# Kernel optimization log

Hardware: AMD Instinct MI355X
Metric: run time of the kernel (lower is better)

The kernel has to match this reference:

```python
import jax, jax.numpy as jnp
import numpy as np

N = 100000
E = 1600000
DIMS = [128, 128, 64]


def _gcn_norm(edge_index, num_nodes):
    # PyG gcn_norm: add self-loops, symmetric normalization D^-1/2 (A+I) D^-1/2
    src, dst = edge_index[0], edge_index[1]
    loop = jnp.arange(num_nodes, dtype=src.dtype)
    src = jnp.concatenate([src, loop])
    dst = jnp.concatenate([dst, loop])
    deg = jax.ops.segment_sum(jnp.ones_like(src, dtype=jnp.float32), dst,
                              num_segments=num_nodes)
    dinv = jnp.where(deg > 0, jax.lax.rsqrt(deg), 0.0)
    w = dinv[src] * dinv[dst]  # [E+N]
    return src, dst, w


def _gcn_conv(x, src, dst, w, W, b):
    # transform first (cheaper when out_dim <= in_dim), then aggregate
    h = x @ W                                   # [N, out]
    msg = h[src] * w[:, None]                   # gather + scale  [E+N, out]
    out = jax.ops.segment_sum(msg, dst, num_segments=x.shape[0])
    return out + b


def setup_inputs() -> dict:
    key = jax.random.key(0)
    ks = jax.random.split(key, 6)
    x = jax.random.normal(ks[0], (N, DIMS[0]), dtype=jnp.float32)
    edge_index = jax.random.randint(ks[1], (2, E), 0, N, dtype=jnp.int64)
    # Glorot-style init for GCNConv weights, zero bias (PyG default)
    W1 = jax.random.normal(ks[2], (DIMS[0], DIMS[1]), dtype=jnp.float32) / np.sqrt(DIMS[0])
    b1 = jnp.zeros((DIMS[1],), dtype=jnp.float32)
    W2 = jax.random.normal(ks[3], (DIMS[1], DIMS[2]), dtype=jnp.float32) / np.sqrt(DIMS[1])
    b2 = jnp.zeros((DIMS[2],), dtype=jnp.float32)
    return {"x": x, "edge_index": edge_index, "W1": W1, "b1": b1, "W2": W2, "b2": b2}


def reference(x, edge_index, W1, b1, W2, b2):
    src, dst, w = _gcn_norm(edge_index, x.shape[0])
    h = _gcn_conv(x, src, dst, w, W1, b1)
    h = jax.nn.relu(h)
    # dropout is identity in eval mode (deterministic reference)
    out = _gcn_conv(h, src, dst, w, W2, b2)
    return out
```

## Files before the change

### kernel.cpp

```cpp
#include <hip/hip_runtime.h>
#include <hip/hip_fp16.h>

#define TPB 256
#define CHUNK 1024
#define EPB 4096
#define CSHIFT 8

typedef _Float16 half8 __attribute__((ext_vector_type(8)));
typedef float    f32x4 __attribute__((ext_vector_type(4)));


__global__ __launch_bounds__(256) void scanA_kernel(const int* __restrict__ cnt,
                                                    int* __restrict__ row_ptr,
                                                    int* __restrict__ chunk_sums, int n) {
    __shared__ int ls[256];
    const int t    = threadIdx.x;
    const int base = blockIdx.x * CHUNK;
    const int idx  = base + t * 4;
    int4 v = make_int4(0, 0, 0, 0);
    if (idx + 3 < n) v = *(const int4*)(cnt + idx);
    else {
        if (idx + 0 < n) v.x = cnt[idx + 0];
        if (idx + 1 < n) v.y = cnt[idx + 1];
        if (idx + 2 < n) v.z = cnt[idx + 2];
        if (idx + 3 < n) v.w = cnt[idx + 3];
    }
    int s0 = v.x, s1 = s0 + v.y, s2 = s1 + v.z, s3 = s2 + v.w;
    ls[t] = s3;
    __syncthreads();
    for (int off = 1; off < 256; off <<= 1) {
        int xv = (t >= off) ? ls[t - off] : 0;
        __syncthreads();
        ls[t] += xv;
        __syncthreads();
    }
    int excl = (t == 0) ? 0 : ls[t - 1];
    if (idx + 0 < n) row_ptr[idx + 0] = excl;
    if (idx + 1 < n) row_ptr[idx + 1] = excl + s0;
    if (idx + 2 < n) row_ptr[idx + 2] = excl + s1;
    if (idx + 3 < n) row_ptr[idx + 3] = excl + s2;
    if (t == 255) chunk_sums[blockIdx.x] = ls[255];
}

__global__ __launch_bounds__(256) void scanB_kernel(int* __restrict__ chunk_sums, int nch) {
    __shared__ int ls[256];
    const int t = threadIdx.x;
    ls[t] = (t < nch) ? chunk_sums[t] : 0;
    __syncthreads();
    for (int off = 1; off < 256; off <<= 1) {
        int xv = (t >= off) ? ls[t - off] : 0;
        __syncthreads();
        ls[t] += xv;
        __syncthreads();
    }
    if (t < nch) chunk_sums[t] = (t == 0) ? 0 : ls[t - 1];
}

__global__ __launch_bounds__(256) void scanC_kernel(int* __restrict__ row_ptr,
                                                    const int* __restrict__ chunk_sums, int n) {
    const int base = blockIdx.x * CHUNK;
    const int off  = chunk_sums[blockIdx.x];
    for (int k = threadIdx.x; k < CHUNK; k += 256) {
        int i = base + k;
        if (i < n) row_ptr[i] += off;
    }
}


__global__ __launch_bounds__(256) void hist_kernel(const int* __restrict__ dst,
                                                   int* __restrict__ hist_g,
                                                   int e, int nbc, int nblk) {
    __shared__ int hs[512];
    const int t = threadIdx.x;
    for (int i = t; i < nbc; i += 256) hs[i] = 0;
    __syncthreads();
    const int e0  = blockIdx.x * EPB;
    const int lim = min(e0 + EPB, e);
    for (int i = e0 + t; i < lim; i += 256)
        atomicAdd(&hs[dst[i] >> CSHIFT], 1);
    __syncthreads();
    for (int b = t; b < nbc; b += 256)
        hist_g[b * nblk + blockIdx.x] = hs[b];
}

__global__ __launch_bounds__(256) void partition_kernel(const int* __restrict__ src,
                                                        const int* __restrict__ dst,
                                                        const int* __restrict__ hist_scan,
                                                        int* __restrict__ pairs,
                                                        int e, int nbc, int nblk) {
    __shared__ int  hs[512];
    __shared__ int  lscan[512];
    __shared__ int  lfill[512];
    __shared__ int  base_s[512];
    __shared__ int  ls[256];
    __shared__ int2 sp[EPB];
    const int t = threadIdx.x;
    for (int i = t; i < nbc; i += 256) { hs[i] = 0; lfill[i] = 0; }
    __syncthreads();
    const int e0  = blockIdx.x * EPB;
    const int lim = min(e0 + EPB, e);
    for (int i = e0 + t; i < lim; i += 256)
        atomicAdd(&hs[dst[i] >> CSHIFT], 1);
    __syncthreads();
    int v0 = (2 * t     < nbc) ? hs[2 * t]     : 0;
    int v1 = (2 * t + 1 < nbc) ? hs[2 * t + 1] : 0;
    ls[t] = v0 + v1;
    __syncthreads();
    for (int off = 1; off < 256; off <<= 1) {
        int xv = (t >= off) ? ls[t - off] : 0;
        __syncthreads();
        ls[t] += xv;
        __syncthreads();
    }
    int excl = (t == 0) ? 0 : ls[t - 1];
    if (2 * t     < nbc) lscan[2 * t]     = excl;
    if (2 * t + 1 < nbc) lscan[2 * t + 1] = excl + v0;
    for (int b = t; b < nbc; b += 256) base_s[b] = hist_scan[b * nblk + blockIdx.x];
    __syncthreads();
    for (int i = e0 + t; i < lim; i += 256) {
        int d = dst[i];
        int b = d >> CSHIFT;
        int r = atomicAdd(&lfill[b], 1);
        sp[lscan[b] + r] = make_int2(src[i], d);
    }
    __syncthreads();
    const int cnt = lim - e0;
    for (int i = t; i < cnt; i += 256) {
        int2 pr = sp[i];
        int  b  = pr.y >> CSHIFT;
        pairs[base_s[b] + (i - lscan[b])] = pr.x | ((pr.y & 255) << 17);
    }
}

__global__ __launch_bounds__(256) void bucket_finalize_kernel(const int* __restrict__ pairs,
                                                              const int* __restrict__ hist_scan,
                                                              int* __restrict__ row_ptr,
                                                              float* __restrict__ dinv,
                                                              int* __restrict__ csr_src,
                                                              int n, int e, int nbc, int nblk) {
    __shared__ int cnt_s[256];
    __shared__ int fill[256];
    __shared__ int ls[256];
    const int b   = blockIdx.x;
    const int nb0 = b << CSHIFT;
    const int t   = threadIdx.x;
    const int r0  = hist_scan[b * nblk];
    const int r1  = (b + 1 < nbc) ? hist_scan[(b + 1) * nblk] : e;
    cnt_s[t] = 0;
    __syncthreads();
    for (int i = r0 + t; i < r1; i += 256)
        atomicAdd(&cnt_s[pairs[i] >> 17], 1);
    __syncthreads();
    int c = cnt_s[t];
    ls[t] = c;
    __syncthreads();
    for (int off = 1; off < 256; off <<= 1) {
        int xv = (t >= off) ? ls[t - off] : 0;
        __syncthreads();
        ls[t] += xv;
        __syncthreads();
    }
    int excl = (t == 0) ? 0 : ls[t - 1];
    int node = nb0 + t;
    if (node < n) {
        row_ptr[node] = r0 + excl;
        dinv[node]    = rsqrtf((float)(c + 1));
    }
    fill[t] = r0 + excl;
    __syncthreads();
    for (int i = r0 + t; i < r1; i += 256) {
        int pr = pairs[i];
        int p  = atomicAdd(&fill[pr >> 17], 1);
        csr_src[p] = pr & 0x1FFFF;
    }
    if (b == 0 && t == 0) row_ptr[n] = e;
}


template <int M, bool RELU, typename XT>
__global__ __launch_bounds__(256) void gemm_mfma_kernel(const XT* __restrict__ X,
                                                        const float* __restrict__ W,
                                                        const float* __restrict__ dinv,
                                                        __half* __restrict__ H, int nrows) {
    constexpr int NC = M / 16;
    __shared__ __align__(16) _Float16 Wf[NC * 4 * 64 * 8];

    const int tid = threadIdx.x;

    for (int f = tid; f < NC * 4 * 64; f += 256) {
        int c    = f >> 8;
        int i    = (f >> 6) & 3;
        int lane = f & 63;
        int quad = lane >> 4, n = lane & 15;
        const float* wp = W + (size_t)(i * 32 + quad * 8) * M + c * 16 + n;
        half8 hv;
#pragma unroll
        for (int j = 0; j < 8; ++j) hv[j] = (_Float16)wp[(size_t)j * M];
        ((half8*)Wf)[f] = hv;
    }
    __syncthreads();

    const int  wave = tid >> 6, lane = tid & 63;
    const int  quad = lane >> 4, n16 = lane & 15;
    const long rowbase = (long)blockIdx.x * 64 + wave * 16;

    long arow = rowbase + n16;
    const XT* xrow = X + (size_t)(arow < nrows ? arow : 0) * 128;
    half8 a[4];
    if constexpr (sizeof(XT) == 4) {
        const float4* xr = (const float4*)xrow;
#pragma unroll
        for (int i = 0; i < 4; ++i) {
            float4 x0 = xr[i * 8 + quad * 2];
            float4 x1 = xr[i * 8 + quad * 2 + 1];
            if (RELU) {
                x0.x = fmaxf(x0.x, 0.f); x0.y = fmaxf(x0.y, 0.f);
                x0.z = fmaxf(x0.z, 0.f); x0.w = fmaxf(x0.w, 0.f);
                x1.x = fmaxf(x1.x, 0.f); x1.y = fmaxf(x1.y, 0.f);
                x1.z = fmaxf(x1.z, 0.f); x1.w = fmaxf(x1.w, 0.f);
            }
            half8 hv;
            hv[0] = (_Float16)x0.x; hv[1] = (_Float16)x0.y;
            hv[2] = (_Float16)x0.z; hv[3] = (_Float16)x0.w;
            hv[4] = (_Float16)x1.x; hv[5] = (_Float16)x1.y;
            hv[6] = (_Float16)x1.z; hv[7] = (_Float16)x1.w;
            a[i] = hv;
        }
    } else {
        const half8* xr = (const half8*)xrow;
#pragma unroll
        for (int i = 0; i < 4; ++i) {
            half8 hv = xr[i * 4 + quad];
            if (RELU) {
#pragma unroll
                for (int j = 0; j < 8; ++j)
                    hv[j] = (hv[j] > (_Float16)0) ? hv[j] : (_Float16)0;
            }
            a[i] = hv;
        }
    }

    float dv[4];
#pragma unroll
    for (int r = 0; r < 4; ++r) {
        long orow = rowbase + quad * 4 + r;
        dv[r] = (orow < nrows) ? dinv[orow] : 0.f;
    }

    for (int c = 0; c < NC; ++c) {
        f32x4 acc = {0.f, 0.f, 0.f, 0.f};
#pragma unroll
        for (int i = 0; i < 4; ++i) {
            half8 b = ((const half8*)Wf)[(c * 4 + i) * 64 + lane];
            acc = __builtin_amdgcn_mfma_f32_16x16x32_f16(a[i], b, acc, 0, 0, 0);
        }
#pragma unroll
        for (int r = 0; r < 4; ++r) {
            long orow = rowbase + quad * 4 + r;
            if (orow < nrows)
                H[orow * M + c * 16 + n16] = __float2half(acc[r] * dv[r]);
        }
    }
}


__global__ __launch_bounds__(TPB) void agg_pull128_kernel(const __half* __restrict__ hs,
                                                          const int* __restrict__ csr_src,
                                                          const int* __restrict__ row_ptr,
                                                          const float* __restrict__ dinv,
                                                          const float* __restrict__ bias,
                                                          __half* __restrict__ out, int n) {
    const int node = blockIdx.x * (TPB / 64) + (threadIdx.x >> 6);
    const int lane = threadIdx.x & 63;
    if (node >= n) return;
    const int beg = row_ptr[node];
    const int end = row_ptr[node + 1];

    const __half2* hp = (const __half2*)hs;
    float2 a[16];
#pragma unroll
    for (int r = 1; r < 16; ++r) a[r] = make_float2(0.f, 0.f);
    a[0] = __half22float2(hp[(long)node * 64 + lane]);
    for (int base = beg; base < end; base += 64) {
        int m = end - base; if (m > 64) m = 64;
        int idx = (lane < m) ? csr_src[base + lane] : 0;
        int j = 0;
        for (; j + 16 <= m; j += 16) {
#pragma unroll
            for (int r = 0; r < 16; ++r) {
                int s = __shfl(idx, j + r);
                float2 v = __half22float2(hp[(long)s * 64 + lane]);
                a[r].x += v.x; a[r].y += v.y;
            }
        }
        for (; j + 4 <= m; j += 4) {
#pragma unroll
            for (int r = 0; r < 4; ++r) {
                int s = __shfl(idx, j + r);
                float2 v = __half22float2(hp[(long)s * 64 + lane]);
                a[r].x += v.x; a[r].y += v.y;
            }
        }
        for (; j < m; ++j) {
            int s = __shfl(idx, j);
            float2 v = __half22float2(hp[(long)s * 64 + lane]);
            a[0].x += v.x; a[0].y += v.y;
        }
    }
#pragma unroll
    for (int r = 8; r < 16; ++r) { a[r - 8].x += a[r].x; a[r - 8].y += a[r].y; }
#pragma unroll
    for (int r = 4; r < 8; ++r) { a[r - 4].x += a[r].x; a[r - 4].y += a[r].y; }
    float  di = dinv[node];
    float2 bv = ((const float2*)bias)[lane];
    float ox = bv.x + di * ((a[0].x + a[1].x) + (a[2].x + a[3].x));
    float oy = bv.y + di * ((a[0].y + a[1].y) + (a[2].y + a[3].y));
    ((__half2*)out)[(long)node * 64 + lane] = __floats2half2_rn(ox, oy);
}


__global__ __launch_bounds__(TPB) void agg_pull64_kernel(const __half* __restrict__ hs,
                                                         const int* __restrict__ csr_src,
                                                         const int* __restrict__ row_ptr,
                                                         const float* __restrict__ dinv,
                                                         const float* __restrict__ bias,
                                                         float* __restrict__ out, int n) {
    const int node = blockIdx.x * (TPB / 64) + (threadIdx.x >> 6);
    const int lane = threadIdx.x & 63;
    if (node >= n) return;
    const int half = lane >> 5;
    const int sl   = lane & 31;
    const int beg = row_ptr[node];
    const int end = row_ptr[node + 1];
    const __half2* hp = (const __half2*)hs;

    float2 a[8];
#pragma unroll
    for (int r = 0; r < 8; ++r) a[r] = make_float2(0.f, 0.f);

    for (int base = beg; base < end; base += 64) {
        int m = end - base; if (m > 64) m = 64;
        int idx = (lane < m) ? csr_src[base + lane] : 0;
        int j = 0;
        for (; j + 16 <= m; j += 16) {
#pragma unroll
            for (int r = 0; r < 8; ++r) {
                int s = __shfl(idx, j + 2 * r + half);
                float2 v = __half22float2(hp[(long)s * 32 + sl]);
                a[r].x += v.x; a[r].y += v.y;
            }
        }
        for (; j + 2 <= m; j += 2) {
            int s = __shfl(idx, j + half);
            float2 v = __half22float2(hp[(long)s * 32 + sl]);
            a[0].x += v.x; a[0].y += v.y;
        }
        if (j < m) {
            int s = __shfl(idx, j);
            float2 v = __half22float2(hp[(long)s * 32 + sl]);
            if (half == 0) { a[0].x += v.x; a[0].y += v.y; }
        }
    }
#pragma unroll
    for (int r = 4; r < 8; ++r) { a[r - 4].x += a[r].x; a[r - 4].y += a[r].y; }
    float2 acc;
    acc.x = (a[0].x + a[1].x) + (a[2].x + a[3].x);
    acc.y = (a[0].y + a[1].y) + (a[2].y + a[3].y);
    acc.x += __shfl(acc.x, lane ^ 32);
    acc.y += __shfl(acc.y, lane ^ 32);
    if (half == 0) {
        float2 sv = __half22float2(hp[(long)node * 32 + sl]);
        float  di = dinv[node];
        float2 bv = ((const float2*)bias)[sl];
        float2 o;
        o.x = bv.x + di * (acc.x + sv.x);
        o.y = bv.y + di * (acc.y + sv.y);
        ((float2*)out)[(long)node * 32 + sl] = o;
    }
}


extern "C" void kernel_launch(void* const* d_in, const int* in_sizes, int n_in,
                              void* d_out, int out_size, void* d_ws, size_t ws_size,
                              hipStream_t stream) {
    const float* x  = (const float*)d_in[0];
    const int*   ei = (const int*)d_in[1];
    const float* W1 = (const float*)d_in[2];
    const float* b1 = (const float*)d_in[3];
    const float* W2 = (const float*)d_in[4];
    const float* b2 = (const float*)d_in[5];
    float* out = (float*)d_out;

    const int N = in_sizes[0] / 128;
    const int E = in_sizes[1] / 2;
    const int* srcv = ei;
    const int* dstv = ei + E;

    const int NBC    = (N + 255) >> CSHIFT;
    const int NBLK_E = (E + EPB - 1) / EPB;
    const int HLEN   = NBC * NBLK_E;
    const int NCHH   = (HLEN + CHUNK - 1) / CHUNK;

    char* p = (char*)d_ws;
    int*    row_ptr    = (int*)p;           p += ((size_t)N + 64) * 4;
    int*    chunk_sums = (int*)p;           p += 1024;
    int*    hist       = (int*)p;           p += ((size_t)HLEN + 64) * 4;
    int*    csr_src    = (int*)p;           p += (size_t)E * 4;
    float*  dinv       = (float*)p;         p += ((size_t)N + 64) * 4;
    __half* hs1        = (__half*)p;        p += (size_t)N * 128 * 2;
    __half* out1       = (__half*)p;        p += (size_t)N * 128 * 2;
    int*    pairs      = (int*)out1;
    __half* hs2        = hs1;

    hist_kernel<<<NBLK_E, 256, 0, stream>>>(dstv, hist, E, NBC, NBLK_E);
    scanA_kernel<<<NCHH, 256, 0, stream>>>(hist, hist, chunk_sums, HLEN);
    scanB_kernel<<<1, 256, 0, stream>>>(chunk_sums, NCHH);
    scanC_kernel<<<NCHH, 256, 0, stream>>>(hist, chunk_sums, HLEN);
    partition_kernel<<<NBLK_E, 256, 0, stream>>>(srcv, dstv, hist, pairs, E, NBC, NBLK_E);
    bucket_finalize_kernel<<<NBC, 256, 0, stream>>>(pairs, hist, row_ptr, dinv, csr_src,
                                                    N, E, NBC, NBLK_E);

    gemm_mfma_kernel<128, false, float><<<(N + 63) / 64, 256, 0, stream>>>(x, W1, dinv, hs1, N);
    agg_pull128_kernel<<<(N + 3) / 4, TPB, 0, stream>>>(hs1, csr_src, row_ptr, dinv, b1, out1, N);

    gemm_mfma_kernel<64, true, _Float16><<<(N + 63) / 64, 256, 0, stream>>>(
        (const _Float16*)out1, W2, dinv, hs2, N);
    agg_pull64_kernel<<<(N + 3) / 4, TPB, 0, stream>>>(hs2, csr_src, row_ptr, dinv, b2, out, N);
}
```

Measured before the change: 308.3 us.

## Widen CSR build buckets to 512 nodes and fold chunk scan into scanC

```diff
diff --git a/kernel.cpp b/kernel.cpp
--- a/kernel.cpp
+++ b/kernel.cpp
@@ -4,7 +4,7 @@
 #define TPB 256
 #define CHUNK 1024
 #define EPB 4096
-#define CSHIFT 8
+#define CSHIFT 9
 
 typedef _Float16 half8 __attribute__((ext_vector_type(8)));
 typedef float    f32x4 __attribute__((ext_vector_type(4)));
@@ -42,7 +42,10 @@
     if (t == 255) chunk_sums[blockIdx.x] = ls[255];
 }
 
-__global__ __launch_bounds__(256) void scanB_kernel(int* __restrict__ chunk_sums, int nch) {
+
+__global__ __launch_bounds__(256) void scanC_kernel(int* __restrict__ row_ptr,
+                                                    const int* __restrict__ chunk_sums,
+                                                    int n, int nch) {
     __shared__ int ls[256];
     const int t = threadIdx.x;
     ls[t] = (t < nch) ? chunk_sums[t] : 0;
@@ -53,16 +56,11 @@
         ls[t] += xv;
         __syncthreads();
     }
-    if (t < nch) chunk_sums[t] = (t == 0) ? 0 : ls[t - 1];
-}
-
-__global__ __launch_bounds__(256) void scanC_kernel(int* __restrict__ row_ptr,
-                                                    const int* __restrict__ chunk_sums, int n) {
+    const int boff = (blockIdx.x == 0) ? 0 : ls[blockIdx.x - 1];
     const int base = blockIdx.x * CHUNK;
-    const int off  = chunk_sums[blockIdx.x];
-    for (int k = threadIdx.x; k < CHUNK; k += 256) {
+    for (int k = t; k < CHUNK; k += 256) {
         int i = base + k;
-        if (i < n) row_ptr[i] += off;
+        if (i < n) row_ptr[i] += boff;
     }
 }
 
@@ -70,17 +68,16 @@
 __global__ __launch_bounds__(256) void hist_kernel(const int* __restrict__ dst,
                                                    int* __restrict__ hist_g,
                                                    int e, int nbc, int nblk) {
-    __shared__ int hs[512];
+    __shared__ int hs[256];
     const int t = threadIdx.x;
-    for (int i = t; i < nbc; i += 256) hs[i] = 0;
+    if (t < nbc) hs[t] = 0;
     __syncthreads();
     const int e0  = blockIdx.x * EPB;
     const int lim = min(e0 + EPB, e);
     for (int i = e0 + t; i < lim; i += 256)
         atomicAdd(&hs[dst[i] >> CSHIFT], 1);
     __syncthreads();
-    for (int b = t; b < nbc; b += 256)
-        hist_g[b * nblk + blockIdx.x] = hs[b];
+    if (t < nbc) hist_g[t * nblk + blockIdx.x] = hs[t];
 }
 
 __global__ __launch_bounds__(256) void partition_kernel(const int* __restrict__ src,
@@ -88,23 +85,21 @@
                                                         const int* __restrict__ hist_scan,
                                                         int* __restrict__ pairs,
                                                         int e, int nbc, int nblk) {
-    __shared__ int  hs[512];
-    __shared__ int  lscan[512];
-    __shared__ int  lfill[512];
-    __shared__ int  base_s[512];
+    __shared__ int  hs[256];
+    __shared__ int  lscan[256];
+    __shared__ int  lfill[256];
+    __shared__ int  base_s[256];
     __shared__ int  ls[256];
     __shared__ int2 sp[EPB];
     const int t = threadIdx.x;
-    for (int i = t; i < nbc; i += 256) { hs[i] = 0; lfill[i] = 0; }
+    if (t < nbc) { hs[t] = 0; lfill[t] = 0; }
     __syncthreads();
     const int e0  = blockIdx.x * EPB;
     const int lim = min(e0 + EPB, e);
     for (int i = e0 + t; i < lim; i += 256)
         atomicAdd(&hs[dst[i] >> CSHIFT], 1);
     __syncthreads();
-    int v0 = (2 * t     < nbc) ? hs[2 * t]     : 0;
-    int v1 = (2 * t + 1 < nbc) ? hs[2 * t + 1] : 0;
-    ls[t] = v0 + v1;
+    ls[t] = (t < nbc) ? hs[t] : 0;
     __syncthreads();
     for (int off = 1; off < 256; off <<= 1) {
         int xv = (t >= off) ? ls[t - off] : 0;
@@ -112,10 +107,10 @@
         ls[t] += xv;
         __syncthreads();
     }
-    int excl = (t == 0) ? 0 : ls[t - 1];
-    if (2 * t     < nbc) lscan[2 * t]     = excl;
-    if (2 * t + 1 < nbc) lscan[2 * t + 1] = excl + v0;
-    for (int b = t; b < nbc; b += 256) base_s[b] = hist_scan[b * nblk + blockIdx.x];
+    if (t < nbc) {
+        lscan[t]  = (t == 0) ? 0 : ls[t - 1];
+        base_s[t] = hist_scan[t * nblk + blockIdx.x];
+    }
     __syncthreads();
     for (int i = e0 + t; i < lim; i += 256) {
         int d = dst[i];
@@ -128,7 +123,7 @@
     for (int i = t; i < cnt; i += 256) {
         int2 pr = sp[i];
         int  b  = pr.y >> CSHIFT;
-        pairs[base_s[b] + (i - lscan[b])] = pr.x | ((pr.y & 255) << 17);
+        pairs[base_s[b] + (i - lscan[b])] = pr.x | ((pr.y & 511) << 17);
     }
 }
 
@@ -138,21 +133,22 @@
                                                               float* __restrict__ dinv,
                                                               int* __restrict__ csr_src,
                                                               int n, int e, int nbc, int nblk) {
-    __shared__ int cnt_s[256];
-    __shared__ int fill[256];
+    __shared__ int cnt_s[512];
+    __shared__ int fill[512];
     __shared__ int ls[256];
     const int b   = blockIdx.x;
     const int nb0 = b << CSHIFT;
     const int t   = threadIdx.x;
     const int r0  = hist_scan[b * nblk];
     const int r1  = (b + 1 < nbc) ? hist_scan[(b + 1) * nblk] : e;
-    cnt_s[t] = 0;
+    cnt_s[t] = 0; cnt_s[t + 256] = 0;
     __syncthreads();
     for (int i = r0 + t; i < r1; i += 256)
         atomicAdd(&cnt_s[pairs[i] >> 17], 1);
     __syncthreads();
-    int c = cnt_s[t];
-    ls[t] = c;
+    int v0 = cnt_s[2 * t];
+    int v1 = cnt_s[2 * t + 1];
+    ls[t] = v0 + v1;
     __syncthreads();
     for (int off = 1; off < 256; off <<= 1) {
         int xv = (t >= off) ? ls[t - off] : 0;
@@ -161,12 +157,20 @@
         __syncthreads();
     }
     int excl = (t == 0) ? 0 : ls[t - 1];
-    int node = nb0 + t;
-    if (node < n) {
-        row_ptr[node] = r0 + excl;
-        dinv[node]    = rsqrtf((float)(c + 1));
-    }
-    fill[t] = r0 + excl;
+    int off0 = r0 + excl;
+    int off1 = off0 + v0;
+    int node0 = nb0 + 2 * t;
+    int node1 = nb0 + 2 * t + 1;
+    if (node0 < n) {
+        row_ptr[node0] = off0;
+        dinv[node0]    = rsqrtf((float)(v0 + 1));
+    }
+    if (node1 < n) {
+        row_ptr[node1] = off1;
+        dinv[node1]    = rsqrtf((float)(v1 + 1));
+    }
+    fill[2 * t]     = off0;
+    fill[2 * t + 1] = off1;
     __syncthreads();
     for (int i = r0 + t; i < r1; i += 256) {
         int pr = pairs[i];
@@ -396,7 +400,7 @@
     const int* srcv = ei;
     const int* dstv = ei + E;
 
-    const int NBC    = (N + 255) >> CSHIFT;
+    const int NBC    = (N + 511) >> CSHIFT;
     const int NBLK_E = (E + EPB - 1) / EPB;
     const int HLEN   = NBC * NBLK_E;
     const int NCHH   = (HLEN + CHUNK - 1) / CHUNK;
@@ -414,8 +418,7 @@
 
     hist_kernel<<<NBLK_E, 256, 0, stream>>>(dstv, hist, E, NBC, NBLK_E);
     scanA_kernel<<<NCHH, 256, 0, stream>>>(hist, hist, chunk_sums, HLEN);
-    scanB_kernel<<<1, 256, 0, stream>>>(chunk_sums, NCHH);
-    scanC_kernel<<<NCHH, 256, 0, stream>>>(hist, chunk_sums, HLEN);
+    scanC_kernel<<<NCHH, 256, 0, stream>>>(hist, chunk_sums, HLEN, NCHH);
     partition_kernel<<<NBLK_E, 256, 0, stream>>>(srcv, dstv, hist, pairs, E, NBC, NBLK_E);
     bucket_finalize_kernel<<<NBC, 256, 0, stream>>>(pairs, hist, row_ptr, dinv, csr_src,
                                                     N, E, NBC, NBLK_E);
```

Measured after the change: 310.3 us. Within noise of the previous version (+0.7%).
